# Optimization experiments

Measured on AMD Instinct MI355X. Metric: run time of the kernel, lower is better.

The kernel has to match this reference:

```python
import jax, jax.numpy as jnp
import numpy as np

N_E = 1024
E_DIM = 64
BETA = 0.25


def setup_inputs() -> dict:
    key = jax.random.key(0)
    k1, k2 = jax.random.split(key)
    z = jax.random.normal(k1, (16, E_DIM, 64, 64), dtype=jnp.float32)
    # embedding initialized uniform(-1/n_e, 1/n_e) as in the torch module
    emb = jax.random.uniform(k2, (N_E, E_DIM), dtype=jnp.float32,
                             minval=-1.0 / N_E, maxval=1.0 / N_E)
    return {"z": z, "emb": emb}


def reference(z, emb):
    n_e, e_dim = emb.shape
    # NCHW -> NHWC, flatten to tokens
    zp = jnp.transpose(z, (0, 2, 3, 1))            # [B,H,W,C]
    zf = zp.reshape(-1, e_dim)                      # [N,C]
    # squared distances ||zf||^2 + ||e||^2 - 2 zf e^T  -> [N, n_e]
    d = (jnp.sum(zf * zf, axis=1, keepdims=True)
         + jnp.sum(emb * emb, axis=1)
         - 2.0 * jnp.matmul(zf, emb.T))
    idx = jnp.argmin(d, axis=1)                     # [N]
    # one-hot @ emb is exactly a gather
    z_q = emb[idx].reshape(zp.shape)                # [B,H,W,C]
    loss = (jnp.mean((jax.lax.stop_gradient(z_q) - zp) ** 2)
            + BETA * jnp.mean((z_q - jax.lax.stop_gradient(zp)) ** 2))
    # straight-through estimator
    z_q = zp + jax.lax.stop_gradient(z_q - zp)
    # perplexity from codeword usage histogram
    counts = jax.ops.segment_sum(jnp.ones_like(idx, dtype=zf.dtype), idx,
                                 num_segments=n_e)
    e_mean = counts / zf.shape[0]
    perplexity = jnp.exp(-jnp.sum(e_mean * jnp.log(e_mean + 1e-10)))
    min_encoding_indices = idx.reshape(z.shape[0], -1).astype(jnp.int32)
    z_q = jnp.transpose(z_q, (0, 3, 1, 2))          # back to NCHW
    return z_q, loss, perplexity, min_encoding_indices
```

## Files before the change

### kernel.cpp

```cpp
#include <hip/hip_runtime.h>

#define TOKS 65536
#define ED 64
#define NE 1024
#define CH_STRIDE 4096
#define B_STRIDE 262144

typedef __bf16 bf16x8 __attribute__((ext_vector_type(8)));
typedef float f32x16 __attribute__((ext_vector_type(16)));
typedef unsigned short ushort_t;
typedef unsigned int uint_t;


__device__ __forceinline__ ushort_t f2bf(float x) {
    uint_t u = __float_as_uint(x);
    uint_t r = u + 0x7FFFu + ((u >> 16) & 1u);
    return (ushort_t)(r >> 16);
}

__global__ __launch_bounds__(256) void vq_prep_e(const float* __restrict__ emb,
                                                 ushort_t* __restrict__ efrag,
                                                 float* __restrict__ enorm,
                                                 int* __restrict__ hist) {
    const int tid = threadIdx.x;
    const int w = tid >> 6, lane = tid & 63;
    const int j = blockIdx.x * 4 + w;

    const float e = emb[j * 64 + lane];
    const float sq = __fmul_rn(e, e);
    float acc = sq;
    acc = __fadd_rn(acc, __shfl_down(sq, 8, 64));
    acc = __fadd_rn(acc, __shfl_down(sq, 16, 64));
    acc = __fadd_rn(acc, __shfl_down(sq, 24, 64));
    acc = __fadd_rn(acc, __shfl_down(sq, 32, 64));
    acc = __fadd_rn(acc, __shfl_down(sq, 40, 64));
    acc = __fadd_rn(acc, __shfl_down(sq, 48, 64));
    acc = __fadd_rn(acc, __shfl_down(sq, 56, 64));
    float x = __fadd_rn(acc, __shfl_down(acc, 1, 64));
    float y = __fadd_rn(x, __shfl_down(x, 2, 64));
    float zn = __fadd_rn(y, __shfl_down(y, 4, 64));
    if (lane == 0) enorm[j] = zn;

    const ushort_t h = f2bf(-2.0f * e);
    const int ct = j >> 5, m = j & 31;
    const int ks = lane >> 4, kh = (lane >> 3) & 1, i = lane & 7;
    efrag[(size_t)((ct * 4 + ks) * 512) + (m + 32 * kh) * 8 + i] = h;

    if (blockIdx.x < 4) hist[blockIdx.x * 256 + tid] = 0;
}

__global__ __launch_bounds__(256, 4) void vq_main(
    const float* __restrict__ z,
    const ushort_t* __restrict__ efrag,
    const float* __restrict__ enorm,
    const float* __restrict__ emb,
    float* __restrict__ zq,
    float* __restrict__ out_idx,
    int* __restrict__ hist,
    double* __restrict__ lossPart) {
    __shared__ float z_s[64][68];
    __shared__ uint_t skey[4][2][32][2][2];
    __shared__ float s_zn[64];
    __shared__ unsigned long long s_res[64];
    __shared__ uint_t s_cand[256];
    __shared__ int s_cnt;
    __shared__ double wsum[4];

    const int tid = threadIdx.x;
    const int w = tid >> 6, lane = tid & 63;
    const int t0 = blockIdx.x * 64;
    const int b = t0 >> 12, hw0 = t0 & 4095;
    const float* zbase = z + (size_t)b * B_STRIDE + hw0;

    {
        const int c = tid >> 2, u0 = (tid & 3) * 16;
        const float* src = zbase + (size_t)c * CH_STRIDE + u0;
        float4 f0 = *(const float4*)(src);
        float4 f1 = *(const float4*)(src + 4);
        float4 f2 = *(const float4*)(src + 8);
        float4 f3 = *(const float4*)(src + 12);
        float4* dst = (float4*)&z_s[c][u0];
        dst[0] = f0; dst[1] = f1; dst[2] = f2; dst[3] = f3;
    }
    if (tid < 64) s_res[tid] = 0xFFFFFFFFFFFFFFFFull;
    if (tid == 0) s_cnt = 0;

    const int n = lane & 31, kh = lane >> 5;

    bf16x8 zbA[4], zbB[4];
    #pragma unroll
    for (int ks = 0; ks < 4; ++ks) {
        #pragma unroll
        for (int i = 0; i < 8; ++i) {
            const size_t off = (size_t)(ks * 16 + kh * 8 + i) * CH_STRIDE;
            union { ushort_t u; __bf16 bh; } ca, cb;
            ca.u = f2bf(zbase[off + n]);
            cb.u = f2bf(zbase[off + 32 + n]);
            zbA[ks][i] = ca.bh;
            zbB[ks][i] = cb.bh;
        }
    }

    uint_t kA0 = 0xFFFFFFFFu, kA1 = 0xFFFFFFFFu;
    uint_t kB0 = 0xFFFFFFFFu, kB1 = 0xFFFFFFFFu;
    const bf16x8* eg = (const bf16x8*)efrag;

    bf16x8 ah0 = eg[(size_t)((w * 8) * 4 + 0) * 64 + lane];
    bf16x8 ah1 = eg[(size_t)((w * 8) * 4 + 1) * 64 + lane];
    bf16x8 ah2 = eg[(size_t)((w * 8) * 4 + 2) * 64 + lane];
    bf16x8 ah3 = eg[(size_t)((w * 8) * 4 + 3) * 64 + lane];

    for (int ct = 0; ct < 8; ++ct) {
        const int gct = w * 8 + ct;
        bf16x8 nx0, nx1, nx2, nx3;
        if (ct < 7) {
            nx0 = eg[(size_t)((gct + 1) * 4 + 0) * 64 + lane];
            nx1 = eg[(size_t)((gct + 1) * 4 + 1) * 64 + lane];
            nx2 = eg[(size_t)((gct + 1) * 4 + 2) * 64 + lane];
            nx3 = eg[(size_t)((gct + 1) * 4 + 3) * 64 + lane];
        }
        const int jb = gct * 32 + 4 * kh;

        f32x16 accA;
        #pragma unroll
        for (int r = 0; r < 16; ++r) accA[r] = 0.25f;
        accA = __builtin_amdgcn_mfma_f32_32x32x16_bf16(ah0, zbA[0], accA, 0, 0, 0);
        accA = __builtin_amdgcn_mfma_f32_32x32x16_bf16(ah1, zbA[1], accA, 0, 0, 0);
        accA = __builtin_amdgcn_mfma_f32_32x32x16_bf16(ah2, zbA[2], accA, 0, 0, 0);
        accA = __builtin_amdgcn_mfma_f32_32x32x16_bf16(ah3, zbA[3], accA, 0, 0, 0);

        f32x16 accB;
        #pragma unroll
        for (int r = 0; r < 16; ++r) accB[r] = 0.25f;
        accB = __builtin_amdgcn_mfma_f32_32x32x16_bf16(ah0, zbB[0], accB, 0, 0, 0);
        accB = __builtin_amdgcn_mfma_f32_32x32x16_bf16(ah1, zbB[1], accB, 0, 0, 0);
        accB = __builtin_amdgcn_mfma_f32_32x32x16_bf16(ah2, zbB[2], accB, 0, 0, 0);
        accB = __builtin_amdgcn_mfma_f32_32x32x16_bf16(ah3, zbB[3], accB, 0, 0, 0);

        #pragma unroll
        for (int r = 0; r < 16; ++r) {
            const uint_t jbits = (uint_t)(jb + (r & 3) + 8 * (r >> 2));
            uint_t keyA = (__float_as_uint(accA[r]) & 0xFFFFFC00u) | jbits;
            uint_t mxA = max(kA0, keyA);
            kA1 = min(kA1, mxA);
            kA0 = min(kA0, keyA);
            uint_t keyB = (__float_as_uint(accB[r]) & 0xFFFFFC00u) | jbits;
            uint_t mxB = max(kB0, keyB);
            kB1 = min(kB1, mxB);
            kB0 = min(kB0, keyB);
        }
        ah0 = nx0; ah1 = nx1; ah2 = nx2; ah3 = nx3;
    }

    skey[w][0][n][kh][0] = kA0; skey[w][0][n][kh][1] = kA1;
    skey[w][1][n][kh][0] = kB0; skey[w][1][n][kh][1] = kB1;
    __syncthreads();

    const int t_loc = tid >> 2, m = tid & 3;
    const int tile = t_loc >> 5, nn = t_loc & 31;
    {
        uint_t ck[4];
        ck[0] = skey[m][tile][nn][0][0];
        ck[1] = skey[m][tile][nn][0][1];
        ck[2] = skey[m][tile][nn][1][0];
        ck[3] = skey[m][tile][nn][1][1];
        uint_t kmin = min(min(ck[0], ck[1]), min(ck[2], ck[3]));
        kmin = min(kmin, (uint_t)__shfl_xor((int)kmin, 1, 64));
        kmin = min(kmin, (uint_t)__shfl_xor((int)kmin, 2, 64));
        const float thr = __uint_as_float(kmin & 0xFFFFFC00u) + 4.0e-4f;
        #pragma unroll
        for (int s = 0; s < 4; ++s) {
            if (__uint_as_float(ck[s] & 0xFFFFFC00u) <= thr) {
                int pos = atomicAdd(&s_cnt, 1);
                if (pos < 256)
                    s_cand[pos] = ((uint_t)t_loc << 10) | (ck[s] & 1023u);
            }
        }
    }
    {
        float a0 = z_s[m][t_loc];
        float ra = __fmul_rn(a0, a0);
        float b0 = z_s[m + 4][t_loc];
        float rb = __fmul_rn(b0, b0);
        #pragma unroll
        for (int i = 1; i < 8; ++i) {
            float av = z_s[m + 8 * i][t_loc];
            ra = __fadd_rn(ra, __fmul_rn(av, av));
            float bv = z_s[m + 4 + 8 * i][t_loc];
            rb = __fadd_rn(rb, __fmul_rn(bv, bv));
        }
        float xa = __fadd_rn(ra, __shfl_xor(ra, 1, 64));
        float A = __fadd_rn(xa, __shfl_xor(xa, 2, 64));
        float xb = __fadd_rn(rb, __shfl_xor(rb, 1, 64));
        float B = __fadd_rn(xb, __shfl_xor(xb, 2, 64));
        if (m == 0) s_zn[t_loc] = __fadd_rn(A, B);
    }
    __syncthreads();

    {
        const int cnt = s_cnt;
        if (tid < cnt && tid < 256) {
            const uint_t cd = s_cand[tid];
            const int tok = (int)(cd >> 10), j = (int)(cd & 1023u);
            const float* e = emb + (size_t)j * 64;
            float a0 = 0.f;
            #pragma unroll
            for (int k4 = 0; k4 < 64; k4 += 4) {
                float4 e4 = *(const float4*)(e + k4);
                a0 = __fmaf_rn(z_s[k4 + 0][tok], e4.x, a0);
                a0 = __fmaf_rn(z_s[k4 + 1][tok], e4.y, a0);
                a0 = __fmaf_rn(z_s[k4 + 2][tok], e4.z, a0);
                a0 = __fmaf_rn(z_s[k4 + 3][tok], e4.w, a0);
            }
            float d = __fsub_rn(__fadd_rn(s_zn[tok], enorm[j]), 2.0f * a0);
            unsigned long long key =
                ((unsigned long long)__float_as_uint(d) << 10)
                | (unsigned long long)j;
            atomicMin(&s_res[tok], key);
        }
    }
    __syncthreads();

    const int bj = (int)(s_res[t_loc] & 1023u);
    if (m == 0) {
        out_idx[t0 + t_loc] = (float)bj;
        atomicAdd(&hist[bj], 1);
    }
    double ls = 0.0;
    {
        const float* e = emb + (size_t)bj * 64;
        #pragma unroll
        for (int i = 0; i < 16; ++i) {
            const int k = m + 4 * i;
            float ev = e[k];
            float zv = z_s[k][t_loc];
            z_s[k][t_loc] = ev;
            float df = ev - zv;
            ls += (double)(df * df);
        }
    }
    #pragma unroll
    for (int off = 32; off > 0; off >>= 1) ls += __shfl_down(ls, off, 64);
    if (lane == 0) wsum[w] = ls;
    __syncthreads();
    if (tid == 0)
        lossPart[blockIdx.x] = wsum[0] + wsum[1] + wsum[2] + wsum[3];

    {
        const int c = tid >> 2, u0 = (tid & 3) * 16;
        const float4* s4 = (const float4*)&z_s[c][u0];
        float4 f0 = s4[0], f1 = s4[1], f2 = s4[2], f3 = s4[3];
        float* dst = zq + (size_t)b * B_STRIDE + (size_t)c * CH_STRIDE + hw0 + u0;
        *(float4*)(dst) = f0;
        *(float4*)(dst + 4) = f1;
        *(float4*)(dst + 8) = f2;
        *(float4*)(dst + 12) = f3;
    }
}

__global__ __launch_bounds__(256) void vq_final(const int* __restrict__ hist,
                                                const double* __restrict__ lossPart,
                                                float* __restrict__ outs) {
    __shared__ double red[256];
    __shared__ double red2[256];
    double acc = 0.0;
    for (int j = threadIdx.x; j < NE; j += 256) {
        double em = (double)hist[j] * (1.0 / 65536.0);
        acc += em * log(em + 1e-10);
    }
    double lsum = 0.0;
    for (int j = threadIdx.x; j < 1024; j += 256) lsum += lossPart[j];
    red[threadIdx.x] = acc;
    red2[threadIdx.x] = lsum;
    __syncthreads();
    for (int s = 128; s > 0; s >>= 1) {
        if (threadIdx.x < s) {
            red[threadIdx.x] += red[threadIdx.x + s];
            red2[threadIdx.x] += red2[threadIdx.x + s];
        }
        __syncthreads();
    }
    if (threadIdx.x == 0) {
        outs[0] = (float)(1.25 * red2[0] * (1.0 / 4194304.0));
        outs[1] = (float)exp(-red[0]);
    }
}

extern "C" void kernel_launch(void* const* d_in, const int* in_sizes, int n_in,
                              void* d_out, int out_size, void* d_ws, size_t ws_size,
                              hipStream_t stream) {
    const float* z = (const float*)d_in[0];
    const float* emb = (const float*)d_in[1];
    float* out = (float*)d_out;

    char* ws = (char*)d_ws;
    ushort_t* efrag = (ushort_t*)ws;
    float* enorm = (float*)(ws + 131072);
    int* hist = (int*)(ws + 135168);
    double* lossPart = (double*)(ws + 143360);

    float* zq = out;
    float* scalars = out + 4194304;
    float* out_idx = out + 4194306;

    vq_prep_e<<<256, 256, 0, stream>>>(emb, efrag, enorm, hist);
    vq_main<<<1024, 256, 0, stream>>>(z, efrag, enorm, emb, zq, out_idx, hist, lossPart);
    vq_final<<<1, 256, 0, stream>>>(hist, lossPart, scalars);
}
```

Before: 47.91 us.

## Transpose z tile in LDS to token-major and rotate codebook chunk order per block

The shared z tile is now stored token-major with a padded row of 72. The MFMA B-operand fragments are built from vectorized LDS reads instead of 64 strided global loads per thread. The refine, norm and loss/gather phases switch to float4 LDS accesses along the channel axis. The codebook chunk traversal is rotated by blockIdx to spread efrag reads across different addresses. In exchange, the initial store and the final writeback become scalar transposing LDS accesses, and an extra __syncthreads is added before fragment construction.

```diff
diff --git a/kernel.cpp b/kernel.cpp
--- a/kernel.cpp
+++ b/kernel.cpp
@@ -58,7 +58,7 @@
     float* __restrict__ out_idx,
     int* __restrict__ hist,
     double* __restrict__ lossPart) {
-    __shared__ float z_s[64][68];
+    __shared__ float z_s[64][72];
     __shared__ uint_t skey[4][2][32][2][2];
     __shared__ float s_zn[64];
     __shared__ unsigned long long s_res[64];
@@ -79,23 +79,35 @@
         float4 f1 = *(const float4*)(src + 4);
         float4 f2 = *(const float4*)(src + 8);
         float4 f3 = *(const float4*)(src + 12);
-        float4* dst = (float4*)&z_s[c][u0];
-        dst[0] = f0; dst[1] = f1; dst[2] = f2; dst[3] = f3;
+        z_s[u0 +  0][c] = f0.x; z_s[u0 +  1][c] = f0.y;
+        z_s[u0 +  2][c] = f0.z; z_s[u0 +  3][c] = f0.w;
+        z_s[u0 +  4][c] = f1.x; z_s[u0 +  5][c] = f1.y;
+        z_s[u0 +  6][c] = f1.z; z_s[u0 +  7][c] = f1.w;
+        z_s[u0 +  8][c] = f2.x; z_s[u0 +  9][c] = f2.y;
+        z_s[u0 + 10][c] = f2.z; z_s[u0 + 11][c] = f2.w;
+        z_s[u0 + 12][c] = f3.x; z_s[u0 + 13][c] = f3.y;
+        z_s[u0 + 14][c] = f3.z; z_s[u0 + 15][c] = f3.w;
     }
     if (tid < 64) s_res[tid] = 0xFFFFFFFFFFFFFFFFull;
     if (tid == 0) s_cnt = 0;
+    __syncthreads();
 
     const int n = lane & 31, kh = lane >> 5;
 
     bf16x8 zbA[4], zbB[4];
     #pragma unroll
     for (int ks = 0; ks < 4; ++ks) {
+        float4 a0 = *(const float4*)&z_s[n][ks * 16 + kh * 8];
+        float4 a1 = *(const float4*)&z_s[n][ks * 16 + kh * 8 + 4];
+        float4 b0 = *(const float4*)&z_s[32 + n][ks * 16 + kh * 8];
+        float4 b1 = *(const float4*)&z_s[32 + n][ks * 16 + kh * 8 + 4];
+        const float av[8] = {a0.x, a0.y, a0.z, a0.w, a1.x, a1.y, a1.z, a1.w};
+        const float bv[8] = {b0.x, b0.y, b0.z, b0.w, b1.x, b1.y, b1.z, b1.w};
         #pragma unroll
         for (int i = 0; i < 8; ++i) {
-            const size_t off = (size_t)(ks * 16 + kh * 8 + i) * CH_STRIDE;
             union { ushort_t u; __bf16 bh; } ca, cb;
-            ca.u = f2bf(zbase[off + n]);
-            cb.u = f2bf(zbase[off + 32 + n]);
+            ca.u = f2bf(av[i]);
+            cb.u = f2bf(bv[i]);
             zbA[ks][i] = ca.bh;
             zbB[ks][i] = cb.bh;
         }
@@ -104,20 +116,22 @@
     uint_t kA0 = 0xFFFFFFFFu, kA1 = 0xFFFFFFFFu;
     uint_t kB0 = 0xFFFFFFFFu, kB1 = 0xFFFFFFFFu;
     const bf16x8* eg = (const bf16x8*)efrag;
-
-    bf16x8 ah0 = eg[(size_t)((w * 8) * 4 + 0) * 64 + lane];
-    bf16x8 ah1 = eg[(size_t)((w * 8) * 4 + 1) * 64 + lane];
-    bf16x8 ah2 = eg[(size_t)((w * 8) * 4 + 2) * 64 + lane];
-    bf16x8 ah3 = eg[(size_t)((w * 8) * 4 + 3) * 64 + lane];
+    const int rot = blockIdx.x & 7;
+
+    int gct = w * 8 + rot;
+    bf16x8 ah0 = eg[(size_t)(gct * 4 + 0) * 64 + lane];
+    bf16x8 ah1 = eg[(size_t)(gct * 4 + 1) * 64 + lane];
+    bf16x8 ah2 = eg[(size_t)(gct * 4 + 2) * 64 + lane];
+    bf16x8 ah3 = eg[(size_t)(gct * 4 + 3) * 64 + lane];
 
     for (int ct = 0; ct < 8; ++ct) {
-        const int gct = w * 8 + ct;
+        const int gnext = w * 8 + ((ct + 1 + rot) & 7);
         bf16x8 nx0, nx1, nx2, nx3;
         if (ct < 7) {
-            nx0 = eg[(size_t)((gct + 1) * 4 + 0) * 64 + lane];
-            nx1 = eg[(size_t)((gct + 1) * 4 + 1) * 64 + lane];
-            nx2 = eg[(size_t)((gct + 1) * 4 + 2) * 64 + lane];
-            nx3 = eg[(size_t)((gct + 1) * 4 + 3) * 64 + lane];
+            nx0 = eg[(size_t)(gnext * 4 + 0) * 64 + lane];
+            nx1 = eg[(size_t)(gnext * 4 + 1) * 64 + lane];
+            nx2 = eg[(size_t)(gnext * 4 + 2) * 64 + lane];
+            nx3 = eg[(size_t)(gnext * 4 + 3) * 64 + lane];
         }
         const int jb = gct * 32 + 4 * kh;
 
@@ -150,6 +164,7 @@
             kB0 = min(kB0, keyB);
         }
         ah0 = nx0; ah1 = nx1; ah2 = nx2; ah3 = nx3;
+        gct = gnext;
     }
 
     skey[w][0][n][kh][0] = kA0; skey[w][0][n][kh][1] = kA1;
@@ -178,15 +193,15 @@
         }
     }
     {
-        float a0 = z_s[m][t_loc];
+        float a0 = z_s[t_loc][m];
         float ra = __fmul_rn(a0, a0);
-        float b0 = z_s[m + 4][t_loc];
+        float b0 = z_s[t_loc][m + 4];
         float rb = __fmul_rn(b0, b0);
         #pragma unroll
         for (int i = 1; i < 8; ++i) {
-            float av = z_s[m + 8 * i][t_loc];
+            float av = z_s[t_loc][m + 8 * i];
             ra = __fadd_rn(ra, __fmul_rn(av, av));
-            float bv = z_s[m + 4 + 8 * i][t_loc];
+            float bv = z_s[t_loc][m + 4 + 8 * i];
             rb = __fadd_rn(rb, __fmul_rn(bv, bv));
         }
         float xa = __fadd_rn(ra, __shfl_xor(ra, 1, 64));
@@ -205,12 +220,13 @@
             const float* e = emb + (size_t)j * 64;
             float a0 = 0.f;
             #pragma unroll
-            for (int k4 = 0; k4 < 64; k4 += 4) {
-                float4 e4 = *(const float4*)(e + k4);
-                a0 = __fmaf_rn(z_s[k4 + 0][tok], e4.x, a0);
-                a0 = __fmaf_rn(z_s[k4 + 1][tok], e4.y, a0);
-                a0 = __fmaf_rn(z_s[k4 + 2][tok], e4.z, a0);
-                a0 = __fmaf_rn(z_s[k4 + 3][tok], e4.w, a0);
+            for (int k4 = 0; k4 < 16; ++k4) {
+                float4 z4 = *(const float4*)&z_s[tok][k4 * 4];
+                float4 e4 = *(const float4*)(e + k4 * 4);
+                a0 = __fmaf_rn(z4.x, e4.x, a0);
+                a0 = __fmaf_rn(z4.y, e4.y, a0);
+                a0 = __fmaf_rn(z4.z, e4.z, a0);
+                a0 = __fmaf_rn(z4.w, e4.w, a0);
             }
             float d = __fsub_rn(__fadd_rn(s_zn[tok], enorm[j]), 2.0f * a0);
             unsigned long long key =
@@ -228,16 +244,36 @@
     }
     double ls = 0.0;
     {
-        const float* e = emb + (size_t)bj * 64;
-        #pragma unroll
-        for (int i = 0; i < 16; ++i) {
-            const int k = m + 4 * i;
-            float ev = e[k];
-            float zv = z_s[k][t_loc];
-            z_s[k][t_loc] = ev;
-            float df = ev - zv;
-            ls += (double)(df * df);
-        }
+        const float* e = emb + (size_t)bj * 64 + m * 16;
+        float4 e0 = *(const float4*)(e);
+        float4 e1 = *(const float4*)(e + 4);
+        float4 e2 = *(const float4*)(e + 8);
+        float4 e3 = *(const float4*)(e + 12);
+        float4 zv0 = *(const float4*)&z_s[t_loc][m * 16];
+        float4 zv1 = *(const float4*)&z_s[t_loc][m * 16 + 4];
+        float4 zv2 = *(const float4*)&z_s[t_loc][m * 16 + 8];
+        float4 zv3 = *(const float4*)&z_s[t_loc][m * 16 + 12];
+        float df;
+        df = e0.x - zv0.x; ls += (double)(df * df);
+        df = e0.y - zv0.y; ls += (double)(df * df);
+        df = e0.z - zv0.z; ls += (double)(df * df);
+        df = e0.w - zv0.w; ls += (double)(df * df);
+        df = e1.x - zv1.x; ls += (double)(df * df);
+        df = e1.y - zv1.y; ls += (double)(df * df);
+        df = e1.z - zv1.z; ls += (double)(df * df);
+        df = e1.w - zv1.w; ls += (double)(df * df);
+        df = e2.x - zv2.x; ls += (double)(df * df);
+        df = e2.y - zv2.y; ls += (double)(df * df);
+        df = e2.z - zv2.z; ls += (double)(df * df);
+        df = e2.w - zv2.w; ls += (double)(df * df);
+        df = e3.x - zv3.x; ls += (double)(df * df);
+        df = e3.y - zv3.y; ls += (double)(df * df);
+        df = e3.z - zv3.z; ls += (double)(df * df);
+        df = e3.w - zv3.w; ls += (double)(df * df);
+        *(float4*)&z_s[t_loc][m * 16] = e0;
+        *(float4*)&z_s[t_loc][m * 16 + 4] = e1;
+        *(float4*)&z_s[t_loc][m * 16 + 8] = e2;
+        *(float4*)&z_s[t_loc][m * 16 + 12] = e3;
     }
     #pragma unroll
     for (int off = 32; off > 0; off >>= 1) ls += __shfl_down(ls, off, 64);
@@ -248,8 +284,15 @@
 
     {
         const int c = tid >> 2, u0 = (tid & 3) * 16;
-        const float4* s4 = (const float4*)&z_s[c][u0];
-        float4 f0 = s4[0], f1 = s4[1], f2 = s4[2], f3 = s4[3];
+        float4 f0, f1, f2, f3;
+        f0.x = z_s[u0 +  0][c]; f0.y = z_s[u0 +  1][c];
+        f0.z = z_s[u0 +  2][c]; f0.w = z_s[u0 +  3][c];
+        f1.x = z_s[u0 +  4][c]; f1.y = z_s[u0 +  5][c];
+        f1.z = z_s[u0 +  6][c]; f1.w = z_s[u0 +  7][c];
+        f2.x = z_s[u0 +  8][c]; f2.y = z_s[u0 +  9][c];
+        f2.z = z_s[u0 + 10][c]; f2.w = z_s[u0 + 11][c];
+        f3.x = z_s[u0 + 12][c]; f3.y = z_s[u0 + 13][c];
+        f3.z = z_s[u0 + 14][c]; f3.w = z_s[u0 + 15][c];
         float* dst = zq + (size_t)b * B_STRIDE + (size_t)c * CH_STRIDE + hw0 + u0;
         *(float4*)(dst) = f0;
         *(float4*)(dst + 4) = f1;
```

Result: faster. 46.13 us (-3.7%).
